# Performance work log

Hardware: AMD Instinct MI355X
Metric: run time of the kernel (lower is better)

## Reference

```python
import math
import jax, jax.numpy as jnp
import numpy as np

B, S, D, H = 2, 2048, 1024, 16
Dh = D // H
EPS = 1e-5


def layernorm(x, g, b):
    mu = jnp.mean(x, axis=-1, keepdims=True)
    var = jnp.mean(jnp.square(x - mu), axis=-1, keepdims=True)
    return (x - mu) * jax.lax.rsqrt(var + EPS) * g + b


def setup_inputs() -> dict:
    key = jax.random.key(0)
    ks = jax.random.split(key, 8)
    sc = 0.02
    return {
        "x": jax.random.normal(ks[0], (B, S, D), jnp.float32),
        # per-head wq weights stacked: [H, D, Dh] (wk/wv are unused in the original)
        "wq_w": jax.random.normal(ks[1], (H, D, Dh), jnp.float32) * sc,
        "wq_b": jnp.zeros((H, Dh), jnp.float32),
        "fc_w": jax.random.normal(ks[2], (D, D), jnp.float32) * sc,
        "fc_b": jnp.zeros((D,), jnp.float32),
        "ln1_g": jnp.ones((D,), jnp.float32),
        "ln1_b": jnp.zeros((D,), jnp.float32),
        "w1": jax.random.normal(ks[3], (D, 4 * D), jnp.float32) * sc,
        "b1": jnp.zeros((4 * D,), jnp.float32),
        "w2": jax.random.normal(ks[4], (4 * D, D), jnp.float32) * sc,
        "b2": jnp.zeros((D,), jnp.float32),
        "ln2_g": jnp.ones((D,), jnp.float32),
        "ln2_b": jnp.zeros((D,), jnp.float32),
    }


def reference(x, wq_w, wq_b, fc_w, fc_b, ln1_g, ln1_b, w1, b1, w2, b2, ln2_g, ln2_b):
    # NOTE: original bug — wq is applied to q, k and v; since q=k=v=x, Q=K=V.
    qh = jnp.einsum("bsd,hde->bhse", x, wq_w) + wq_b[None, :, None, :]  # [B,H,S,Dh]
    scores = jnp.einsum("bhse,bhte->bhst", qh, qh) / math.sqrt(Dh)      # [B,H,S,S]
    attn = jax.nn.softmax(scores, axis=-1)
    ctx = jnp.einsum("bhst,bhte->bhse", attn, qh)                        # [B,H,S,Dh]
    # concat heads along last dim (head h -> columns h*Dh:(h+1)*Dh)
    y = jnp.transpose(ctx, (0, 2, 1, 3)).reshape(B, S, D)
    y = y @ fc_w + fc_b
    y = layernorm(y + x, ln1_g, ln1_b)
    y1 = jax.nn.relu(y @ w1 + b1) @ w2 + b2
    return layernorm(y + y1, ln2_g, ln2_b)
```

## Files before the change

### kernel.cpp

```cpp
#include <hip/hip_runtime.h>
#include <hip/hip_bf16.h>

typedef unsigned short u16;
typedef __bf16 bf16x8 __attribute__((ext_vector_type(8)));
typedef float floatx4 __attribute__((ext_vector_type(4)));

__device__ __forceinline__ float bf2f_u(u16 u) {
    union { unsigned int i; float f; } x; x.i = ((unsigned int)u) << 16; return x.f;
}
__device__ __forceinline__ u16 f2bf_u(float f) {
    union { float f; unsigned int i; } x; x.f = f;
    unsigned int r = x.i + 0x7fffu + ((x.i >> 16) & 1u);
    return (u16)(r >> 16);
}

__device__ __forceinline__ void gl_lds16(const void* g, void* l) {
    __builtin_amdgcn_global_load_lds(
        (const __attribute__((address_space(1))) void*)g,
        (__attribute__((address_space(3))) void*)l, 16, 0, 0);
}

__global__ __launch_bounds__(256) void tobf_k(const float* __restrict__ in,
                                              u16* __restrict__ out) {
    int i = (blockIdx.x * 256 + threadIdx.x) * 8;
    float4 v0 = *(const float4*)&in[i];
    float4 v1 = *(const float4*)&in[i + 4];
    u16 tmp[8] = {f2bf_u(v0.x), f2bf_u(v0.y), f2bf_u(v0.z), f2bf_u(v0.w),
                  f2bf_u(v1.x), f2bf_u(v1.y), f2bf_u(v1.z), f2bf_u(v1.w)};
    *(uint4*)&out[i] = *(const uint4*)tmp;
}

__global__ __launch_bounds__(256) void transpose_bf_k(
    const float* __restrict__ in, u16* __restrict__ out,
    int R, int C, size_t inZ, size_t outZ)
{
    __shared__ u16 T[64][80];
    const float* ip = in + blockIdx.z * inZ;
    u16* op = out + blockIdx.z * outZ;
    const int r0 = blockIdx.y * 64, c0 = blockIdx.x * 64;
    const int t = threadIdx.x;
#pragma unroll
    for (int i = 0; i < 4; i++) {
        int c = t + i * 256;
        int rr = c >> 4, cc = (c & 15) * 4;
        float4 v = *(const float4*)&ip[(size_t)(r0 + rr) * C + c0 + cc];
        T[cc + 0][rr] = f2bf_u(v.x); T[cc + 1][rr] = f2bf_u(v.y);
        T[cc + 2][rr] = f2bf_u(v.z); T[cc + 3][rr] = f2bf_u(v.w);
    }
    __syncthreads();
#pragma unroll
    for (int i = 0; i < 2; i++) {
        int c = t + i * 256;
        int oc = c >> 3, k8 = (c & 7) * 8;
        uint4 v = *(const uint4*)&T[oc][k8];
        *(uint4*)&op[(size_t)(c0 + oc) * R + r0 + k8] = v;
    }
}

__global__ __launch_bounds__(256) void gemm_bt_k(
    const u16* __restrict__ A, const u16* __restrict__ Bt,
    int gm, int gn, int N, int K, int ldb,
    const float* __restrict__ bias, const u16* __restrict__ resid,
    float* __restrict__ out, u16* __restrict__ out_bf, int mode)
{
    __shared__ __align__(16) u16 As[128 * 32];
    __shared__ __align__(16) u16 Bs[128 * 32];

    const int id = blockIdx.x;
    const int xcd = id & 7, s = id >> 3;
    const int bandM = gm >> 2, bandN = gn >> 1;
    const int m0 = ((xcd >> 1) * bandM + (s % bandM)) * 128;
    const int n0 = ((xcd & 1) * bandN + (s / bandM)) * 128;

    const int t = threadIdx.x;
    const int wid = t >> 6, lane = t & 63;
    const int wm = (wid >> 1) * 64, wn = (wid & 1) * 64;
    const int lr = lane & 15, quad = lane >> 4;
    const int srow = lane >> 2, scol = (lane & 3) * 8;

    floatx4 acc[4][4];
#pragma unroll
    for (int i = 0; i < 4; i++)
#pragma unroll
        for (int j = 0; j < 4; j++)
            acc[i][j] = (floatx4){0.f, 0.f, 0.f, 0.f};

    for (int k0 = 0; k0 < K; k0 += 32) {
        __syncthreads();
#pragma unroll
        for (int i = 0; i < 2; i++) {
            int rb = (wid * 2 + i) * 16;
            gl_lds16(&A[(size_t)(m0 + rb + srow) * K + k0 + scol], &As[rb * 32]);
        }
#pragma unroll
        for (int i = 0; i < 2; i++) {
            int rb = (wid * 2 + i) * 16;
            gl_lds16(&Bt[(size_t)(n0 + rb + srow) * ldb + k0 + scol], &Bs[rb * 32]);
        }
        __syncthreads();

        bf16x8 af[4], bfr[4];
#pragma unroll
        for (int i = 0; i < 4; i++)
            af[i] = *(const bf16x8*)&As[(wm + i * 16 + lr) * 32 + quad * 8];
#pragma unroll
        for (int j = 0; j < 4; j++)
            bfr[j] = *(const bf16x8*)&Bs[(wn + j * 16 + lr) * 32 + quad * 8];
#pragma unroll
        for (int i = 0; i < 4; i++)
#pragma unroll
            for (int j = 0; j < 4; j++)
                acc[i][j] = __builtin_amdgcn_mfma_f32_16x16x32_bf16(af[i], bfr[j], acc[i][j], 0, 0, 0);
    }

#pragma unroll
    for (int i = 0; i < 4; i++) {
#pragma unroll
        for (int j = 0; j < 4; j++) {
#pragma unroll
            for (int r = 0; r < 4; r++) {
                int grow = m0 + wm + i * 16 + quad * 4 + r;
                int gcol = n0 + wn + j * 16 + lr;
                float val = acc[i][j][r];
                if (bias) val += bias[gcol];
                if (mode == 0) {
                    int bb = grow >> 11, ss = grow & 2047;
                    int h = gcol >> 6, e = gcol & 63;
                    out_bf[(((size_t)bb * 16 + h) * 2048 + ss) * 64 + e] = f2bf_u(val);
                } else if (mode == 1) {
                    size_t idx = (size_t)grow * N + gcol;
                    out[idx] = val + bf2f_u(resid[idx]);
                } else if (mode == 2) {
                    out_bf[(size_t)grow * N + gcol] = f2bf_u(fmaxf(val, 0.f));
                } else if (mode == 3) {
                    size_t idx = (size_t)grow * N + gcol;
                    out[idx] = out[idx] + val;
                } else {
                    size_t idx = (size_t)grow * N + gcol;
                    out_bf[idx] = f2bf_u(val + bf2f_u(resid[idx]));
                }
            }
        }
    }
}

__global__ __launch_bounds__(256) void gemm_bt64_k(
    const u16* __restrict__ A, const u16* __restrict__ Bt,
    int gm, int gn, int N, int K, int ldb,
    const float* __restrict__ bias, const u16* __restrict__ resid,
    float* __restrict__ out, u16* __restrict__ out_bf, int mode)
{
    __shared__ __align__(16) u16 As[128 * 32];
    __shared__ __align__(16) u16 Bs[64 * 32];

    const int id = blockIdx.x;
    const int xcd = id & 7, s = id >> 3;
    const int bandM = gm >> 2, bandN = gn >> 1;
    const int m0 = ((xcd >> 1) * bandM + (s % bandM)) * 128;
    const int n0 = ((xcd & 1) * bandN + (s / bandM)) * 64;

    const int t = threadIdx.x;
    const int wid = t >> 6, lane = t & 63;
    const int wm = (wid >> 1) * 64, wn = (wid & 1) * 32;
    const int lr = lane & 15, quad = lane >> 4;
    const int srow = lane >> 2, scol = (lane & 3) * 8;

    floatx4 acc[4][2];
#pragma unroll
    for (int i = 0; i < 4; i++)
#pragma unroll
        for (int j = 0; j < 2; j++)
            acc[i][j] = (floatx4){0.f, 0.f, 0.f, 0.f};

    for (int k0 = 0; k0 < K; k0 += 32) {
        __syncthreads();
#pragma unroll
        for (int i = 0; i < 2; i++) {
            int rb = (wid * 2 + i) * 16;
            gl_lds16(&A[(size_t)(m0 + rb + srow) * K + k0 + scol], &As[rb * 32]);
        }
        {
            int rb = wid * 16;
            gl_lds16(&Bt[(size_t)(n0 + rb + srow) * ldb + k0 + scol], &Bs[rb * 32]);
        }
        __syncthreads();

        bf16x8 af[4], bfr[2];
#pragma unroll
        for (int i = 0; i < 4; i++)
            af[i] = *(const bf16x8*)&As[(wm + i * 16 + lr) * 32 + quad * 8];
#pragma unroll
        for (int j = 0; j < 2; j++)
            bfr[j] = *(const bf16x8*)&Bs[(wn + j * 16 + lr) * 32 + quad * 8];
#pragma unroll
        for (int i = 0; i < 4; i++)
#pragma unroll
            for (int j = 0; j < 2; j++)
                acc[i][j] = __builtin_amdgcn_mfma_f32_16x16x32_bf16(af[i], bfr[j], acc[i][j], 0, 0, 0);
    }

#pragma unroll
    for (int i = 0; i < 4; i++) {
#pragma unroll
        for (int j = 0; j < 2; j++) {
#pragma unroll
            for (int r = 0; r < 4; r++) {
                int grow = m0 + wm + i * 16 + quad * 4 + r;
                int gcol = n0 + wn + j * 16 + lr;
                float val = acc[i][j][r];
                if (bias) val += bias[gcol];
                if (mode == 0) {
                    int bb = grow >> 11, ss = grow & 2047;
                    int h = gcol >> 6, e = gcol & 63;
                    out_bf[(((size_t)bb * 16 + h) * 2048 + ss) * 64 + e] = f2bf_u(val);
                } else if (mode == 1) {
                    size_t idx = (size_t)grow * N + gcol;
                    out[idx] = val + bf2f_u(resid[idx]);
                } else if (mode == 2) {
                    out_bf[(size_t)grow * N + gcol] = f2bf_u(fmaxf(val, 0.f));
                } else if (mode == 3) {
                    size_t idx = (size_t)grow * N + gcol;
                    out[idx] = out[idx] + val;
                } else {
                    size_t idx = (size_t)grow * N + gcol;
                    out_bf[idx] = f2bf_u(val + bf2f_u(resid[idx]));
                }
            }
        }
    }
}

#define KST 72
#define PST 68
__global__ __launch_bounds__(256) void attn_mfma_k(const u16* __restrict__ qh,
                                                   u16* __restrict__ ctx)
{
    __shared__ __align__(16) u16 Ks[64][KST];
    __shared__ __align__(16) u16 Vt[64][KST];
    __shared__ __align__(16) u16 Ps[4][2][16][PST];

    const int bh = blockIdx.x >> 4;
    const int qb = blockIdx.x & 15;
    const u16* __restrict__ base = qh + (size_t)bh * (2048 * 64);
    const int t = threadIdx.x, wid = t >> 6, lane = t & 63;
    const int lr = lane & 15, quad = lane >> 4;
    const int q0 = qb * 128 + wid * 16;

    bf16x8 af[2][2];
#pragma unroll
    for (int f = 0; f < 2; f++) {
        af[f][0] = *(const bf16x8*)&base[(size_t)(q0 + f * 64 + lr) * 64 + quad * 8];
        af[f][1] = *(const bf16x8*)&base[(size_t)(q0 + f * 64 + lr) * 64 + quad * 8 + 32];
    }

    floatx4 Of[2][4];
#pragma unroll
    for (int f = 0; f < 2; f++)
#pragma unroll
        for (int dt = 0; dt < 4; dt++) Of[f][dt] = (floatx4){0.f, 0.f, 0.f, 0.f};
    float lsum[2][4] = {{0.f,0.f,0.f,0.f},{0.f,0.f,0.f,0.f}};

    const int src0 = t >> 3;
    const int src1 = (t + 256) >> 3;
    const int scol = (t & 7) * 8;

    uint4 stg[2];
    stg[0] = *(const uint4*)&base[(size_t)src0 * 64 + scol];
    stg[1] = *(const uint4*)&base[(size_t)src1 * 64 + scol];
    {
#pragma unroll
        for (int cc = 0; cc < 2; cc++) {
            int row = cc ? src1 : src0;
            *(uint4*)&Ks[row][scol] = stg[cc];
            const u16* pv = (const u16*)&stg[cc];
#pragma unroll
            for (int i = 0; i < 8; i++) {
                int d = scol + i;
                Vt[d][row ^ (d & 0x38)] = pv[i];
            }
        }
    }

    for (int kt = 0; kt < 2048; kt += 64) {
        __syncthreads();
        const bool pf = (kt + 64) < 2048;
        if (pf) {
            stg[0] = *(const uint4*)&base[(size_t)(kt + 64 + src0) * 64 + scol];
            stg[1] = *(const uint4*)&base[(size_t)(kt + 64 + src1) * 64 + scol];
        }

#pragma unroll
        for (int nt = 0; nt < 4; nt++) {
            bf16x8 b0 = *(const bf16x8*)&Ks[nt * 16 + lr][quad * 8];
            bf16x8 b1 = *(const bf16x8*)&Ks[nt * 16 + lr][quad * 8 + 32];
#pragma unroll
            for (int f = 0; f < 2; f++) {
                floatx4 z = (floatx4){0.f, 0.f, 0.f, 0.f};
                z = __builtin_amdgcn_mfma_f32_16x16x32_bf16(af[f][0], b0, z, 0, 0, 0);
                z = __builtin_amdgcn_mfma_f32_16x16x32_bf16(af[f][1], b1, z, 0, 0, 0);
#pragma unroll
                for (int r = 0; r < 4; r++) {
                    float p = __expf(fminf(z[r] * 0.125f, 60.f));
                    lsum[f][r] += p;
                    Ps[wid][f][quad * 4 + r][nt * 16 + lr] = f2bf_u(p);
                }
            }
        }

        bf16x8 aP[2][2];
#pragma unroll
        for (int f = 0; f < 2; f++) {
            aP[f][0] = *(const bf16x8*)&Ps[wid][f][lr][quad * 8];
            aP[f][1] = *(const bf16x8*)&Ps[wid][f][lr][quad * 8 + 32];
        }
#pragma unroll
        for (int dt = 0; dt < 4; dt++) {
            int d = dt * 16 + lr, msk = d & 0x38;
            bf16x8 b0 = *(const bf16x8*)&Vt[d][(quad * 8) ^ msk];
            bf16x8 b1 = *(const bf16x8*)&Vt[d][(32 + quad * 8) ^ msk];
#pragma unroll
            for (int f = 0; f < 2; f++) {
                Of[f][dt] = __builtin_amdgcn_mfma_f32_16x16x32_bf16(aP[f][0], b0, Of[f][dt], 0, 0, 0);
                Of[f][dt] = __builtin_amdgcn_mfma_f32_16x16x32_bf16(aP[f][1], b1, Of[f][dt], 0, 0, 0);
            }
        }

        __syncthreads();
        if (pf) {
#pragma unroll
            for (int cc = 0; cc < 2; cc++) {
                int row = cc ? src1 : src0;
                *(uint4*)&Ks[row][scol] = stg[cc];
                const u16* pv = (const u16*)&stg[cc];
#pragma unroll
                for (int i = 0; i < 8; i++) {
                    int d = scol + i;
                    Vt[d][row ^ (d & 0x38)] = pv[i];
                }
            }
        }
    }

    const int b = bh >> 4, h = bh & 15;
#pragma unroll
    for (int f = 0; f < 2; f++) {
#pragma unroll
        for (int r = 0; r < 4; r++) {
            float l = lsum[f][r];
#pragma unroll
            for (int off = 1; off < 16; off <<= 1) l += __shfl_xor(l, off);
            float inv = 1.f / l;
            size_t rowoff = ((size_t)b * 2048 + q0 + f * 64 + quad * 4 + r) * 1024 + h * 64;
#pragma unroll
            for (int dt = 0; dt < 4; dt++)
                ctx[rowoff + dt * 16 + lr] = f2bf_u(Of[f][dt][r] * inv);
        }
    }
}

__global__ __launch_bounds__(256) void ln_k(const void* __restrict__ in,
                                            const float* __restrict__ g,
                                            const float* __restrict__ b,
                                            float* __restrict__ out_f,
                                            u16* __restrict__ out_bf, int icode)
{
    const int row = blockIdx.x;
    const int t = threadIdx.x;
    float4 v;
    if (icode) {
        v = *(const float4*)&((const float*)in)[(size_t)row * 1024 + t * 4];
    } else {
        ushort4 u = *(const ushort4*)&((const u16*)in)[(size_t)row * 1024 + t * 4];
        v.x = bf2f_u(u.x); v.y = bf2f_u(u.y); v.z = bf2f_u(u.z); v.w = bf2f_u(u.w);
    }
    float s  = v.x + v.y + v.z + v.w;
    float ss = v.x * v.x + v.y * v.y + v.z * v.z + v.w * v.w;
#pragma unroll
    for (int off = 32; off >= 1; off >>= 1) {
        s  += __shfl_down(s, off);
        ss += __shfl_down(ss, off);
    }
    __shared__ float sm[10];
    const int wid = t >> 6, lane = t & 63;
    if (lane == 0) { sm[wid] = s; sm[4 + wid] = ss; }
    __syncthreads();
    if (t == 0) {
        float S  = sm[0] + sm[1] + sm[2] + sm[3];
        float SS = sm[4] + sm[5] + sm[6] + sm[7];
        float mu = S * (1.f / 1024.f);
        float var = SS * (1.f / 1024.f) - mu * mu;
        sm[8] = mu; sm[9] = rsqrtf(fmaxf(var, 0.f) + 1e-5f);
    }
    __syncthreads();
    float mu = sm[8], rs = sm[9];
    float4 G  = *(const float4*)&g[t * 4];
    float4 Bv = *(const float4*)&b[t * 4];
    float r0 = (v.x - mu) * rs * G.x + Bv.x;
    float r1 = (v.y - mu) * rs * G.y + Bv.y;
    float r2 = (v.z - mu) * rs * G.z + Bv.z;
    float r3 = (v.w - mu) * rs * G.w + Bv.w;
    if (out_f) {
        float4 ov = {r0, r1, r2, r3};
        *(float4*)&out_f[(size_t)row * 1024 + t * 4] = ov;
    }
    if (out_bf) {
        ushort4 ou = {f2bf_u(r0), f2bf_u(r1), f2bf_u(r2), f2bf_u(r3)};
        *(ushort4*)&out_bf[(size_t)row * 1024 + t * 4] = ou;
    }
}

extern "C" void kernel_launch(void* const* d_in, const int* in_sizes, int n_in,
                              void* d_out, int out_size, void* d_ws, size_t ws_size,
                              hipStream_t stream)
{
    const float* x    = (const float*)d_in[0];
    const float* wq_w = (const float*)d_in[1];
    const float* wq_b = (const float*)d_in[2];
    const float* fc_w = (const float*)d_in[3];
    const float* fc_b = (const float*)d_in[4];
    const float* ln1g = (const float*)d_in[5];
    const float* ln1b = (const float*)d_in[6];
    const float* w1   = (const float*)d_in[7];
    const float* b1   = (const float*)d_in[8];
    const float* w2   = (const float*)d_in[9];
    const float* b2   = (const float*)d_in[10];
    const float* ln2g = (const float*)d_in[11];
    const float* ln2b = (const float*)d_in[12];

    char* ws = (char*)d_ws;
    const size_t MB = 1024 * 1024;
    u16*   w1_bt  = (u16*)(ws);
    u16*   w2_bt  = (u16*)(ws + 8 * MB);
    u16*   wqm_bt = (u16*)(ws + 16 * MB);
    u16*   fcw_bt = (u16*)(ws + 18 * MB);
    u16*   x_bf   = (u16*)(ws + 20 * MB);
    u16*   qh     = (u16*)(ws + 28 * MB);
    u16*   yln1   = (u16*)(ws + 28 * MB);
    u16*   ctx    = (u16*)(ws + 36 * MB);
    u16*   yfc_bf = (u16*)(ws + 44 * MB);
    u16*   h1     = (u16*)(ws + 36 * MB);
    float* z      = (float*)d_out;
    const bool fullN = ws_size >= 69 * MB;

    transpose_bf_k<<<dim3(64, 16), 256, 0, stream>>>(w1, w1_bt, 1024, 4096, 0, 0);
    transpose_bf_k<<<dim3(16, 64), 256, 0, stream>>>(w2, w2_bt, 4096, 1024, 0, 0);
    transpose_bf_k<<<dim3(1, 16, 16), 256, 0, stream>>>(wq_w, wqm_bt, 1024, 64,
                                                        (size_t)1024 * 64, (size_t)64 * 1024);
    transpose_bf_k<<<dim3(16, 16), 256, 0, stream>>>(fc_w, fcw_bt, 1024, 1024, 0, 0);
    tobf_k<<<2048, 256, 0, stream>>>(x, x_bf);

    gemm_bt64_k<<<512, 256, 0, stream>>>(x_bf, wqm_bt, 32, 16, 1024, 1024, 1024,
                                         wq_b, nullptr, nullptr, qh, 0);
    attn_mfma_k<<<512, 256, 0, stream>>>(qh, ctx);
    gemm_bt64_k<<<512, 256, 0, stream>>>(ctx, fcw_bt, 32, 16, 1024, 1024, 1024,
                                         fc_b, x_bf, nullptr, yfc_bf, 4);
    ln_k<<<4096, 256, 0, stream>>>(yfc_bf, ln1g, ln1b, nullptr, yln1, 0);

    if (fullN) {
        gemm_bt_k<<<1024, 256, 0, stream>>>(yln1, w1_bt, 32, 32, 4096, 1024, 1024,
                                            b1, nullptr, nullptr, h1, 2);
        gemm_bt64_k<<<512, 256, 0, stream>>>(h1, w2_bt, 32, 16, 1024, 4096, 4096,
                                             b2, yln1, z, nullptr, 1);
    } else {
        gemm_bt_k<<<512, 256, 0, stream>>>(yln1, w1_bt, 32, 16, 2048, 1024, 1024,
                                           b1, nullptr, nullptr, h1, 2);
        gemm_bt64_k<<<512, 256, 0, stream>>>(h1, w2_bt, 32, 16, 1024, 2048, 4096,
                                             b2, yln1, z, nullptr, 1);
        gemm_bt_k<<<512, 256, 0, stream>>>(yln1, w1_bt + (size_t)2048 * 1024, 32, 16,
                                           2048, 1024, 1024,
                                           b1 + 2048, nullptr, nullptr, h1, 2);
        gemm_bt64_k<<<512, 256, 0, stream>>>(h1, w2_bt + 2048, 32, 16, 1024, 2048, 4096,
                                             nullptr, nullptr, z, nullptr, 3);
    }
    ln_k<<<4096, 256, 0, stream>>>(z, ln2g, ln2b, (float*)d_out, nullptr, 1);
}
```

Baseline: 446.9 us.

## Double-buffer gemm_bt64 LDS tiles with BK=64 and XOR swizzle

```diff
diff --git a/kernel.cpp b/kernel.cpp
--- a/kernel.cpp
+++ b/kernel.cpp
@@ -150,8 +150,8 @@
     const float* __restrict__ bias, const u16* __restrict__ resid,
     float* __restrict__ out, u16* __restrict__ out_bf, int mode)
 {
-    __shared__ __align__(16) u16 As[128 * 32];
-    __shared__ __align__(16) u16 Bs[64 * 32];
+    __shared__ __align__(16) u16 As[2][128 * 64];
+    __shared__ __align__(16) u16 Bs[2][64 * 64];
 
     const int id = blockIdx.x;
     const int xcd = id & 7, s = id >> 3;
@@ -163,7 +163,8 @@
     const int wid = t >> 6, lane = t & 63;
     const int wm = (wid >> 1) * 64, wn = (wid & 1) * 32;
     const int lr = lane & 15, quad = lane >> 4;
-    const int srow = lane >> 2, scol = (lane & 3) * 8;
+    const int srow = lane >> 3;
+    const int scol = ((lane & 7) ^ (lane >> 3)) * 8;
 
     floatx4 acc[4][2];
 #pragma unroll
@@ -172,31 +173,50 @@
         for (int j = 0; j < 2; j++)
             acc[i][j] = (floatx4){0.f, 0.f, 0.f, 0.f};
 
-    for (int k0 = 0; k0 < K; k0 += 32) {
+    auto stage = [&](int b, int k0) {
+#pragma unroll
+        for (int i = 0; i < 4; i++) {
+            int rb = wid * 32 + i * 8;
+            gl_lds16(&A[(size_t)(m0 + rb + srow) * K + k0 + scol], &As[b][rb * 64]);
+        }
+#pragma unroll
+        for (int i = 0; i < 2; i++) {
+            int rb = wid * 16 + i * 8;
+            gl_lds16(&Bt[(size_t)(n0 + rb + srow) * ldb + k0 + scol], &Bs[b][rb * 64]);
+        }
+    };
+
+    stage(0, 0);
+    __syncthreads();
+
+    int cur = 0;
+    for (int k0 = 0; k0 < K; k0 += 64) {
+        if (k0 + 64 < K) stage(cur ^ 1, k0 + 64);
+
+#pragma unroll
+        for (int kk = 0; kk < 2; kk++) {
+            bf16x8 af[4], bfr[2];
+#pragma unroll
+            for (int i = 0; i < 4; i++) {
+                int R = wm + i * 16 + lr;
+                int c = ((kk * 4 + quad) ^ (lr & 7)) * 8;
+                af[i] = *(const bf16x8*)&As[cur][R * 64 + c];
+            }
+#pragma unroll
+            for (int j = 0; j < 2; j++) {
+                int R = wn + j * 16 + lr;
+                int c = ((kk * 4 + quad) ^ (lr & 7)) * 8;
+                bfr[j] = *(const bf16x8*)&Bs[cur][R * 64 + c];
+            }
+#pragma unroll
+            for (int i = 0; i < 4; i++)
+#pragma unroll
+                for (int j = 0; j < 2; j++)
+                    acc[i][j] = __builtin_amdgcn_mfma_f32_16x16x32_bf16(af[i], bfr[j], acc[i][j], 0, 0, 0);
+        }
+
         __syncthreads();
-#pragma unroll
-        for (int i = 0; i < 2; i++) {
-            int rb = (wid * 2 + i) * 16;
-            gl_lds16(&A[(size_t)(m0 + rb + srow) * K + k0 + scol], &As[rb * 32]);
-        }
-        {
-            int rb = wid * 16;
-            gl_lds16(&Bt[(size_t)(n0 + rb + srow) * ldb + k0 + scol], &Bs[rb * 32]);
-        }
-        __syncthreads();
-
-        bf16x8 af[4], bfr[2];
-#pragma unroll
-        for (int i = 0; i < 4; i++)
-            af[i] = *(const bf16x8*)&As[(wm + i * 16 + lr) * 32 + quad * 8];
-#pragma unroll
-        for (int j = 0; j < 2; j++)
-            bfr[j] = *(const bf16x8*)&Bs[(wn + j * 16 + lr) * 32 + quad * 8];
-#pragma unroll
-        for (int i = 0; i < 4; i++)
-#pragma unroll
-            for (int j = 0; j < 2; j++)
-                acc[i][j] = __builtin_amdgcn_mfma_f32_16x16x32_bf16(af[i], bfr[j], acc[i][j], 0, 0, 0);
+        cur ^= 1;
     }
 
 #pragma unroll
```

Measured after the change: 414.8 us. 1.08x faster.
